# Kernel optimization log

Measured on AMD Instinct MI355X. Metric: run time of the kernel, lower is better.

The kernel has to match this reference:

```python
import jax, jax.numpy as jnp
import numpy as np

K = 3  # Chebyshev order (number of coefficients)


def setup_inputs() -> dict:
    key = jax.random.key(0)
    k1, k2, k3, k4 = jax.random.split(key, 4)
    B, nNode, c_in, T = 16, 512, 32, 64
    c_out = 64
    x = jax.random.normal(k1, (B, nNode, c_in, T), dtype=jnp.float32)
    # scaled Laplacian-like batched adjacency; scale keeps the Chebyshev
    # recursion numerically tame (spectral norm ~ O(1))
    adj = jax.random.normal(k2, (B, nNode, nNode), dtype=jnp.float32) * (1.0 / np.sqrt(nNode))
    # 1x1 conv params: weight [c_out, K*c_in], bias [c_out]
    W = jax.random.normal(k3, (c_out, K * c_in), dtype=jnp.float32) * 0.1
    b = jax.random.normal(k4, (c_out,), dtype=jnp.float32) * 0.1
    return {"x": x, "adj": adj, "W": W, "b": b}


def reference(x, adj, W, b):
    # x: [B, nNode, c_in, T] -> permute(0,2,1,3) -> [B, c_in, nNode, T]
    x = jnp.transpose(x, (0, 2, 1, 3))
    B, c_in, nNode, T = x.shape
    # Chebyshev recursion: L0 = I, L1 = adj, L_k = 2*adj@L_{k-1} - L_{k-2}
    L0 = jnp.broadcast_to(jnp.eye(nNode, dtype=x.dtype), (B, nNode, nNode))
    L1 = adj
    Ls = [L0, L1]
    for _ in range(2, K):
        L2 = 2.0 * jnp.matmul(adj, L1) - L0
        L0, L1 = L1, L2
        Ls.append(L2)
    Lap = jnp.stack(Ls, axis=1)              # [B, K, nNode, nNode]
    Lap = jnp.swapaxes(Lap, -1, -2)          # transpose(-1, -2)
    # einsum 'bcnl,bknq->bckql' then view [B, c_in*K, nNode, T]
    y = jnp.einsum('bcnl,bknq->bckql', x, Lap)  # [B, c_in, K, nNode, T]
    y = y.reshape(B, c_in * K, nNode, T)
    # 1x1 Conv2d: channel mixing + bias
    out = jnp.einsum('oc,bcnl->bonl', W, y) + b[None, :, None, None]
    return out
```

## Files before the change

kernel.cpp:

```cpp
#include <hip/hip_runtime.h>

typedef unsigned short u16;
typedef __bf16 v8bf __attribute__((ext_vector_type(8)));
typedef float f32x4 __attribute__((ext_vector_type(4)));
typedef float f32x16 __attribute__((ext_vector_type(16)));
typedef u16 us8 __attribute__((ext_vector_type(8)));
typedef u16 us4 __attribute__((ext_vector_type(4)));

static __device__ __forceinline__ u16 f2bf(float f) {
  union { __bf16 h; u16 u; } cv;
  cv.h = (__bf16)f;
  return cv.u;
}

static __device__ __forceinline__ void gl_lds16(const u16* g, u16* l) {
  __builtin_amdgcn_global_load_lds(
      (const __attribute__((address_space(1))) unsigned int*)g,
      (__attribute__((address_space(3))) unsigned int*)l, 16, 0, 0);
}

__global__ __launch_bounds__(256)
void prep_k(const float* __restrict__ adj, u16* __restrict__ adjC,
            u16* __restrict__ adjT_bf, const float* __restrict__ x,
            u16* __restrict__ xT, const float* __restrict__ W,
            u16* __restrict__ Mb) {
  const int bid = blockIdx.x;
  const int tid = threadIdx.x;
  __shared__ u16 Ls[64][68];
  if (bid < 1024) {
    const int b = bid >> 6;
    const int r0 = ((bid >> 3) & 7) * 64;
    const int c0 = (bid & 7) * 64;
#pragma unroll
    for (int i = 0; i < 4; ++i) {
      const int idx = tid + 256 * i;
      const int r = idx >> 4;
      const int c4 = (idx & 15) * 4;
      const float4 v = *(const float4*)(adj + ((size_t)(b * 512 + r0 + r) * 512 + c0 + c4));
      us4 o;
      o[0] = f2bf(v.x); o[1] = f2bf(v.y); o[2] = f2bf(v.z); o[3] = f2bf(v.w);
      *(us4*)&Ls[r][c4] = o;
      *(us4*)(adjC + ((size_t)(b * 1024 + r0 + r) * 512 + c0 + c4)) = o;
    }
    __syncthreads();
#pragma unroll
    for (int i = 0; i < 2; ++i) {
      const int idx = tid + 256 * i;
      const int c = idx >> 3;
      const int r8 = (idx & 7) * 8;
      us8 o;
#pragma unroll
      for (int j = 0; j < 8; ++j) o[j] = Ls[r8 + j][c];
      *(us8*)(adjT_bf + ((size_t)(b * 512 + c0 + c) * 512 + r0 + r8)) = o;
    }
  } else if (bid < 5120) {
    const int t = bid - 1024;
    const int b = t >> 8;
    const int q0 = ((t >> 5) & 7) * 64;
    const int j0 = (t & 31) * 64;
#pragma unroll
    for (int i = 0; i < 4; ++i) {
      const int idx = tid + 256 * i;
      const int r = idx >> 4;
      const int j4 = (idx & 15) * 4;
      const float4 v = *(const float4*)(x + ((size_t)(b * 512 + q0 + r) * 2048 + j0 + j4));
      us4 o;
      o[0] = f2bf(v.x); o[1] = f2bf(v.y); o[2] = f2bf(v.z); o[3] = f2bf(v.w);
      *(us4*)&Ls[r][j4] = o;
    }
    __syncthreads();
#pragma unroll
    for (int i = 0; i < 2; ++i) {
      const int idx = tid + 256 * i;
      const int jp = idx >> 3;
      const int q8 = (idx & 7) * 8;
      us8 o;
#pragma unroll
      for (int j = 0; j < 8; ++j) o[j] = Ls[q8 + j][jp];
      *(us8*)(xT + ((size_t)(b * 2048 + j0 + jp) * 512 + q0 + q8)) = o;
    }
  } else {
    for (int i = tid; i < 64 * 96; i += 256) {
      const int cc = i % 96;
      const int r = cc % 3;
      const float w = W[i];
      const float m = (r == 0) ? (w - W[i + 2]) : w;
      Mb[i] = f2bf(m);
    }
  }
}

__global__ __launch_bounds__(256)
void gemm_sq(const u16* __restrict__ adjC_in, const u16* __restrict__ BT,
             u16* __restrict__ adjC) {
  const int b = blockIdx.z;
  const int row0 = blockIdx.y * 128;
  const int col0 = blockIdx.x * 128;
  const u16* Ab = adjC_in + (size_t)b * 1024 * 512;
  const u16* BTb = BT + (size_t)b * 512 * 512;

  __shared__ u16 smem[16384];
  u16* As = smem;
  u16* Bs = smem + 8192;

  const int tid = threadIdx.x;
  const int lane = tid & 63;
  const int w = tid >> 6;
  const int wm = (w >> 1) * 64;
  const int wn = (w & 1) * 64;
  const int l16 = lane & 15;
  const int kg = lane >> 4;

  f32x4 acc[4][4];
#pragma unroll
  for (int m = 0; m < 4; ++m)
#pragma unroll
    for (int n = 0; n < 4; ++n) acc[m][n] = (f32x4){0.f, 0.f, 0.f, 0.f};

  for (int k0 = 0; k0 < 512; k0 += 64) {
    __syncthreads();
#pragma unroll
    for (int i = 0; i < 4; ++i) {
      const int eb = w * 2048 + i * 512;
      const int e = eb + lane * 8;
      const int r = e >> 6;
      const int kk = e & 63;
      gl_lds16(Ab + (size_t)(row0 + r) * 512 + k0 + kk, As + eb);
      gl_lds16(BTb + (size_t)(col0 + r) * 512 + k0 + kk, Bs + eb);
    }
    __syncthreads();
#pragma unroll
    for (int ks = 0; ks < 2; ++ks) {
      v8bf af[4], bfr[4];
#pragma unroll
      for (int m = 0; m < 4; ++m)
        af[m] = *(const v8bf*)(As + (wm + m * 16 + l16) * 64 + ks * 32 + kg * 8);
#pragma unroll
      for (int n = 0; n < 4; ++n)
        bfr[n] = *(const v8bf*)(Bs + (wn + n * 16 + l16) * 64 + ks * 32 + kg * 8);
#pragma unroll
      for (int m = 0; m < 4; ++m)
#pragma unroll
        for (int n = 0; n < 4; ++n)
          acc[m][n] = __builtin_amdgcn_mfma_f32_16x16x32_bf16(af[m], bfr[n], acc[m][n], 0, 0, 0);
    }
  }
  u16* Cb = adjC + (size_t)b * 1024 * 512 + (size_t)512 * 512;
#pragma unroll
  for (int m = 0; m < 4; ++m)
#pragma unroll
    for (int n = 0; n < 4; ++n)
#pragma unroll
      for (int v = 0; v < 4; ++v) {
        const int rr = row0 + wm + m * 16 + kg * 4 + v;
        const int cc = col0 + wn + n * 16 + l16;
        Cb[(size_t)rr * 512 + cc] = f2bf(2.0f * acc[m][n][v]);
      }
}

__global__ __launch_bounds__(512)
void prop_k(const u16* __restrict__ AC, const u16* __restrict__ BT,
            u16* __restrict__ C) {
  const int fid = blockIdx.x + 16 * (blockIdx.y + 4 * blockIdx.z);
  const int wk = (fid & 7) * 128 + (fid >> 3);
  const int b = wk >> 6;
  const int row0 = ((wk >> 4) & 3) * 256;
  const int col0 = (wk & 15) * 128;
  const u16* Ab = AC + (size_t)b * 1024 * 512;
  const u16* BTb = BT + (size_t)b * 2048 * 512;

  __shared__ u16 smem[24576];
  u16* As = smem;
  u16* Bs = smem + 16384;

  const int tid = threadIdx.x;
  const int lane = tid & 63;
  const int w = tid >> 6;
  const int wm = (w >> 1) * 64;
  const int wn = (w & 1) * 64;
  const int l32 = lane & 31;
  const int hk = lane >> 5;
  const int rsw = (l32 & 7) << 3;

  f32x16 acc[2][2];
#pragma unroll
  for (int mi = 0; mi < 2; ++mi)
#pragma unroll
    for (int ni = 0; ni < 2; ++ni)
#pragma unroll
      for (int v = 0; v < 16; ++v) acc[mi][ni][v] = 0.f;

  for (int k0 = 0; k0 < 512; k0 += 64) {
    __syncthreads();
#pragma unroll
    for (int i = 0; i < 4; ++i) {
      const int cb = w * 64 + i * 512;
      const int c = cb + lane;
      const int r = c >> 3;
      const int slot = (c & 7) ^ (r & 7);
      gl_lds16(Ab + (size_t)(row0 + r) * 512 + k0 + slot * 8, As + cb * 8);
    }
#pragma unroll
    for (int i = 0; i < 2; ++i) {
      const int cb = w * 64 + i * 512;
      const int c = cb + lane;
      const int r = c >> 3;
      const int slot = (c & 7) ^ (r & 7);
      gl_lds16(BTb + (size_t)(col0 + r) * 512 + k0 + slot * 8, Bs + cb * 8);
    }
    __syncthreads();
#pragma unroll
    for (int ks = 0; ks < 4; ++ks) {
      v8bf af[2], bf[2];
#pragma unroll
      for (int mi = 0; mi < 2; ++mi) {
        const int row = wm + mi * 32 + l32;
        af[mi] = *(const v8bf*)(As + row * 64 + ((ks * 16 + hk * 8) ^ rsw));
      }
#pragma unroll
      for (int ni = 0; ni < 2; ++ni) {
        const int row = wn + ni * 32 + l32;
        bf[ni] = *(const v8bf*)(Bs + row * 64 + ((ks * 16 + hk * 8) ^ rsw));
      }
#pragma unroll
      for (int mi = 0; mi < 2; ++mi)
#pragma unroll
        for (int ni = 0; ni < 2; ++ni)
          acc[mi][ni] = __builtin_amdgcn_mfma_f32_32x32x16_bf16(af[mi], bf[ni], acc[mi][ni], 0, 0, 0);
    }
  }

  u16* Cb = C + (size_t)b * 1024 * 2048;
#pragma unroll
  for (int mi = 0; mi < 2; ++mi)
#pragma unroll
    for (int ni = 0; ni < 2; ++ni)
#pragma unroll
      for (int r = 0; r < 16; ++r) {
        const int rr = row0 + wm + mi * 32 + (r & 3) + 8 * (r >> 2) + 4 * hk;
        const int cc = col0 + wn + ni * 32 + l32;
        Cb[(size_t)rr * 2048 + cc] = f2bf(acc[mi][ni][r]);
      }
}

__global__ __launch_bounds__(256)
void mix_mfma(const float* __restrict__ x0, const u16* __restrict__ X1Y2,
              const u16* __restrict__ Mb, const float* __restrict__ bias,
              float* __restrict__ out) {
  const int q = blockIdx.x;
  const int b = blockIdx.y;
  __shared__ u16 Vt[64][104];
  __shared__ u16 Ms[64][104];
  const int tid = threadIdx.x;
  const int lane = tid & 63;
  const int w = tid >> 6;
  const int l16 = lane & 15;
  const int kg = lane >> 4;

#pragma unroll
  for (int i = 0; i < 3; ++i) {
    const int idx = tid + 256 * i;
    const int o = idx / 12;
    const int c8 = (idx % 12) * 8;
    *(uint4*)&Ms[o][c8] = *(const uint4*)(Mb + o * 96 + c8);
  }
  const size_t base0 = ((size_t)b * 512 + q) * 2048;
  const size_t base1 = ((size_t)b * 1024 + q) * 2048;
  const size_t base2 = ((size_t)b * 1024 + 512 + q) * 2048;
#pragma unroll
  for (int i = 0; i < 2; ++i) {
    const int idx = tid + 256 * i;
    const int c = idx >> 4;
    const int l0 = (idx & 15) * 4;
    const float4 v = *(const float4*)(x0 + base0 + c * 64 + l0);
    Vt[l0 + 0][3 * c] = f2bf(v.x);
    Vt[l0 + 1][3 * c] = f2bf(v.y);
    Vt[l0 + 2][3 * c] = f2bf(v.z);
    Vt[l0 + 3][3 * c] = f2bf(v.w);
  }
  {
    const int c = tid >> 3;
    const int l0 = (tid & 7) * 8;
    const us8 v1 = *(const us8*)(X1Y2 + base1 + c * 64 + l0);
    const us8 v2 = *(const us8*)(X1Y2 + base2 + c * 64 + l0);
#pragma unroll
    for (int j = 0; j < 8; ++j) {
      Vt[l0 + j][3 * c + 1] = v1[j];
      Vt[l0 + j][3 * c + 2] = v2[j];
    }
  }
  __syncthreads();

  f32x4 acc[4];
#pragma unroll
  for (int n = 0; n < 4; ++n) acc[n] = (f32x4){0.f, 0.f, 0.f, 0.f};
#pragma unroll
  for (int ks = 0; ks < 3; ++ks) {
    const v8bf a = *(const v8bf*)&Ms[w * 16 + l16][ks * 32 + kg * 8];
#pragma unroll
    for (int n = 0; n < 4; ++n) {
      const v8bf bv = *(const v8bf*)&Vt[n * 16 + l16][ks * 32 + kg * 8];
      acc[n] = __builtin_amdgcn_mfma_f32_16x16x32_bf16(a, bv, acc[n], 0, 0, 0);
    }
  }
#pragma unroll
  for (int n = 0; n < 4; ++n)
#pragma unroll
    for (int v = 0; v < 4; ++v) {
      const int o = w * 16 + kg * 4 + v;
      out[(((size_t)b * 64 + o) * 512 + q) * 64 + n * 16 + l16] = acc[n][v] + bias[o];
    }
}

extern "C" void kernel_launch(void* const* d_in, const int* in_sizes, int n_in,
                              void* d_out, int out_size, void* d_ws, size_t ws_size,
                              hipStream_t stream) {
  const float* x   = (const float*)d_in[0];
  const float* adj = (const float*)d_in[1];
  const float* W   = (const float*)d_in[2];
  const float* bia = (const float*)d_in[3];
  float* out = (float*)d_out;

  u16* adjC    = (u16*)d_ws;
  u16* adjT_bf = adjC    + (size_t)16 * 1024 * 512;
  u16* xT      = adjT_bf + (size_t)16 * 512 * 512;
  u16* X1Y2    = xT      + (size_t)16 * 2048 * 512;
  u16* Mb      = X1Y2    + (size_t)16 * 1024 * 2048;

  hipLaunchKernelGGL(prep_k, dim3(5121), dim3(256), 0, stream,
                     adj, adjC, adjT_bf, x, xT, W, Mb);
  hipLaunchKernelGGL(gemm_sq, dim3(4, 4, 16), dim3(256), 0, stream,
                     adjC, adjT_bf, adjC);
  hipLaunchKernelGGL(prop_k, dim3(16, 4, 16), dim3(512), 0, stream,
                     adjC, xT, X1Y2);
  hipLaunchKernelGGL(mix_mfma, dim3(512, 16), dim3(256), 0, stream,
                     x, X1Y2, Mb, bia, out);
}
```

Baseline: 135.8 us.

## Fuse x transpose and bf16 conversion into propagation GEMM B-tile load

Drops the separate prep pass that transposed x into a bf16 xT buffer. prop_k now reads fp32 x directly with strided per-thread loads, converts to bf16 in registers, and writes the swizzled B tile into LDS. This avoids writing and re-reading a 32 MB bf16 intermediate. In exchange the GEMM main loop now issues synchronous strided global loads instead of async global-to-LDS copies, and each x element is reread by the 4 row blocks per batch.

```diff
diff --git a/kernel.cpp b/kernel.cpp
--- a/kernel.cpp
+++ b/kernel.cpp
@@ -21,8 +21,7 @@
 
 __global__ __launch_bounds__(256)
 void prep_k(const float* __restrict__ adj, u16* __restrict__ adjC,
-            u16* __restrict__ adjT_bf, const float* __restrict__ x,
-            u16* __restrict__ xT, const float* __restrict__ W,
+            u16* __restrict__ adjT_bf, const float* __restrict__ W,
             u16* __restrict__ Mb) {
   const int bid = blockIdx.x;
   const int tid = threadIdx.x;
@@ -53,32 +52,6 @@
       for (int j = 0; j < 8; ++j) o[j] = Ls[r8 + j][c];
       *(us8*)(adjT_bf + ((size_t)(b * 512 + c0 + c) * 512 + r0 + r8)) = o;
     }
-  } else if (bid < 5120) {
-    const int t = bid - 1024;
-    const int b = t >> 8;
-    const int q0 = ((t >> 5) & 7) * 64;
-    const int j0 = (t & 31) * 64;
-#pragma unroll
-    for (int i = 0; i < 4; ++i) {
-      const int idx = tid + 256 * i;
-      const int r = idx >> 4;
-      const int j4 = (idx & 15) * 4;
-      const float4 v = *(const float4*)(x + ((size_t)(b * 512 + q0 + r) * 2048 + j0 + j4));
-      us4 o;
-      o[0] = f2bf(v.x); o[1] = f2bf(v.y); o[2] = f2bf(v.z); o[3] = f2bf(v.w);
-      *(us4*)&Ls[r][j4] = o;
-    }
-    __syncthreads();
-#pragma unroll
-    for (int i = 0; i < 2; ++i) {
-      const int idx = tid + 256 * i;
-      const int jp = idx >> 3;
-      const int q8 = (idx & 7) * 8;
-      us8 o;
-#pragma unroll
-      for (int j = 0; j < 8; ++j) o[j] = Ls[q8 + j][jp];
-      *(us8*)(xT + ((size_t)(b * 2048 + j0 + jp) * 512 + q0 + q8)) = o;
-    }
   } else {
     for (int i = tid; i < 64 * 96; i += 256) {
       const int cc = i % 96;
@@ -159,7 +132,7 @@
 }
 
 __global__ __launch_bounds__(512)
-void prop_k(const u16* __restrict__ AC, const u16* __restrict__ BT,
+void prop_k(const u16* __restrict__ AC, const float* __restrict__ X,
             u16* __restrict__ C) {
   const int fid = blockIdx.x + 16 * (blockIdx.y + 4 * blockIdx.z);
   const int wk = (fid & 7) * 128 + (fid >> 3);
@@ -167,7 +140,7 @@
   const int row0 = ((wk >> 4) & 3) * 256;
   const int col0 = (wk & 15) * 128;
   const u16* Ab = AC + (size_t)b * 1024 * 512;
-  const u16* BTb = BT + (size_t)b * 2048 * 512;
+  const float* Xb = X + (size_t)b * 512 * 2048;
 
   __shared__ u16 smem[24576];
   u16* As = smem;
@@ -181,6 +154,8 @@
   const int l32 = lane & 31;
   const int hk = lane >> 5;
   const int rsw = (l32 & 7) << 3;
+  const int jj = tid & 127;
+  const int qg = tid >> 7;
 
   f32x16 acc[2][2];
 #pragma unroll
@@ -202,11 +177,15 @@
     }
 #pragma unroll
     for (int i = 0; i < 2; ++i) {
-      const int cb = w * 64 + i * 512;
-      const int c = cb + lane;
-      const int r = c >> 3;
-      const int slot = (c & 7) ^ (r & 7);
-      gl_lds16(BTb + (size_t)(col0 + r) * 512 + k0 + slot * 8, Bs + cb * 8);
+      const int oct = qg + i * 4;
+      const float* src = Xb + (size_t)(k0 + oct * 8) * 2048 + col0 + jj;
+      float v[8];
+#pragma unroll
+      for (int u = 0; u < 8; ++u) v[u] = src[(size_t)u * 2048];
+      us8 o;
+#pragma unroll
+      for (int u = 0; u < 8; ++u) o[u] = f2bf(v[u]);
+      *(us8*)(Bs + jj * 64 + ((oct ^ (jj & 7)) * 8)) = o;
     }
     __syncthreads();
 #pragma unroll
@@ -323,16 +302,15 @@
 
   u16* adjC    = (u16*)d_ws;
   u16* adjT_bf = adjC    + (size_t)16 * 1024 * 512;
-  u16* xT      = adjT_bf + (size_t)16 * 512 * 512;
-  u16* X1Y2    = xT      + (size_t)16 * 2048 * 512;
+  u16* X1Y2    = adjT_bf + (size_t)16 * 512 * 512;
   u16* Mb      = X1Y2    + (size_t)16 * 1024 * 2048;
 
-  hipLaunchKernelGGL(prep_k, dim3(5121), dim3(256), 0, stream,
-                     adj, adjC, adjT_bf, x, xT, W, Mb);
+  hipLaunchKernelGGL(prep_k, dim3(1025), dim3(256), 0, stream,
+                     adj, adjC, adjT_bf, W, Mb);
   hipLaunchKernelGGL(gemm_sq, dim3(4, 4, 16), dim3(256), 0, stream,
                      adjC, adjT_bf, adjC);
   hipLaunchKernelGGL(prop_k, dim3(16, 4, 16), dim3(512), 0, stream,
-                     adjC, xT, X1Y2);
+                     adjC, x, X1Y2);
   hipLaunchKernelGGL(mix_mfma, dim3(512, 16), dim3(256), 0, stream,
                      x, X1Y2, Mb, bia, out);
 }
```

Result: slower. 149.0 us (+9.7%).

## Overlap adjacency squaring GEMM with x transpose in one launch

Applied to the files above, without the earlier changes.

Moves the x bf16 transpose out of the prep kernel into the same launch as the adj@adj GEMM, so the 256 GEMM blocks and the 4096 transpose blocks run together. Before, the GEMM launch had only 256 blocks and left much of the GPU idle. The prep kernel now handles only the adjacency conversion and weight folding, so it is smaller. The trade-off is that the combined kernel shares one shared-memory size and register budget across both roles, which can hurt occupancy for the transpose blocks.

```diff
diff --git a/kernel.cpp b/kernel.cpp
--- a/kernel.cpp
+++ b/kernel.cpp
@@ -20,10 +20,9 @@
 }
 
 __global__ __launch_bounds__(256)
-void prep_k(const float* __restrict__ adj, u16* __restrict__ adjC,
-            u16* __restrict__ adjT_bf, const float* __restrict__ x,
-            u16* __restrict__ xT, const float* __restrict__ W,
-            u16* __restrict__ Mb) {
+void prep_adj_k(const float* __restrict__ adj, u16* __restrict__ adjC,
+                u16* __restrict__ adjT_bf, const float* __restrict__ W,
+                u16* __restrict__ Mb) {
   const int bid = blockIdx.x;
   const int tid = threadIdx.x;
   __shared__ u16 Ls[64][68];
@@ -53,8 +52,89 @@
       for (int j = 0; j < 8; ++j) o[j] = Ls[r8 + j][c];
       *(us8*)(adjT_bf + ((size_t)(b * 512 + c0 + c) * 512 + r0 + r8)) = o;
     }
-  } else if (bid < 5120) {
-    const int t = bid - 1024;
+  } else {
+    for (int i = tid; i < 64 * 96; i += 256) {
+      const int cc = i % 96;
+      const int r = cc % 3;
+      const float w = W[i];
+      const float m = (r == 0) ? (w - W[i + 2]) : w;
+      Mb[i] = f2bf(m);
+    }
+  }
+}
+
+__global__ __launch_bounds__(256)
+void phase2_k(const u16* __restrict__ adjC_in, const u16* __restrict__ BT,
+              u16* __restrict__ adjC, const float* __restrict__ x,
+              u16* __restrict__ xT) {
+  const int bid = blockIdx.x;
+  const int tid = threadIdx.x;
+  __shared__ u16 smem[16384];
+  if (bid < 256) {
+    const int b = bid >> 4;
+    const int row0 = ((bid >> 2) & 3) * 128;
+    const int col0 = (bid & 3) * 128;
+    const u16* Ab = adjC_in + (size_t)b * 1024 * 512;
+    const u16* BTb = BT + (size_t)b * 512 * 512;
+
+    u16* As = smem;
+    u16* Bs = smem + 8192;
+
+    const int lane = tid & 63;
+    const int w = tid >> 6;
+    const int wm = (w >> 1) * 64;
+    const int wn = (w & 1) * 64;
+    const int l16 = lane & 15;
+    const int kg = lane >> 4;
+
+    f32x4 acc[4][4];
+#pragma unroll
+    for (int m = 0; m < 4; ++m)
+#pragma unroll
+      for (int n = 0; n < 4; ++n) acc[m][n] = (f32x4){0.f, 0.f, 0.f, 0.f};
+
+    for (int k0 = 0; k0 < 512; k0 += 64) {
+      __syncthreads();
+#pragma unroll
+      for (int i = 0; i < 4; ++i) {
+        const int eb = w * 2048 + i * 512;
+        const int e = eb + lane * 8;
+        const int r = e >> 6;
+        const int kk = e & 63;
+        gl_lds16(Ab + (size_t)(row0 + r) * 512 + k0 + kk, As + eb);
+        gl_lds16(BTb + (size_t)(col0 + r) * 512 + k0 + kk, Bs + eb);
+      }
+      __syncthreads();
+#pragma unroll
+      for (int ks = 0; ks < 2; ++ks) {
+        v8bf af[4], bfr[4];
+#pragma unroll
+        for (int m = 0; m < 4; ++m)
+          af[m] = *(const v8bf*)(As + (wm + m * 16 + l16) * 64 + ks * 32 + kg * 8);
+#pragma unroll
+        for (int n = 0; n < 4; ++n)
+          bfr[n] = *(const v8bf*)(Bs + (wn + n * 16 + l16) * 64 + ks * 32 + kg * 8);
+#pragma unroll
+        for (int m = 0; m < 4; ++m)
+#pragma unroll
+          for (int n = 0; n < 4; ++n)
+            acc[m][n] = __builtin_amdgcn_mfma_f32_16x16x32_bf16(af[m], bfr[n], acc[m][n], 0, 0, 0);
+      }
+    }
+    u16* Cb = adjC + (size_t)b * 1024 * 512 + (size_t)512 * 512;
+#pragma unroll
+    for (int m = 0; m < 4; ++m)
+#pragma unroll
+      for (int n = 0; n < 4; ++n)
+#pragma unroll
+        for (int v = 0; v < 4; ++v) {
+          const int rr = row0 + wm + m * 16 + kg * 4 + v;
+          const int cc = col0 + wn + n * 16 + l16;
+          Cb[(size_t)rr * 512 + cc] = f2bf(2.0f * acc[m][n][v]);
+        }
+  } else {
+    u16 (*Ls)[68] = (u16(*)[68])smem;
+    const int t = bid - 256;
     const int b = t >> 8;
     const int q0 = ((t >> 5) & 7) * 64;
     const int j0 = (t & 31) * 64;
@@ -79,83 +159,7 @@
       for (int j = 0; j < 8; ++j) o[j] = Ls[q8 + j][jp];
       *(us8*)(xT + ((size_t)(b * 2048 + j0 + jp) * 512 + q0 + q8)) = o;
     }
-  } else {
-    for (int i = tid; i < 64 * 96; i += 256) {
-      const int cc = i % 96;
-      const int r = cc % 3;
-      const float w = W[i];
-      const float m = (r == 0) ? (w - W[i + 2]) : w;
-      Mb[i] = f2bf(m);
-    }
-  }
-}
-
-__global__ __launch_bounds__(256)
-void gemm_sq(const u16* __restrict__ adjC_in, const u16* __restrict__ BT,
-             u16* __restrict__ adjC) {
-  const int b = blockIdx.z;
-  const int row0 = blockIdx.y * 128;
-  const int col0 = blockIdx.x * 128;
-  const u16* Ab = adjC_in + (size_t)b * 1024 * 512;
-  const u16* BTb = BT + (size_t)b * 512 * 512;
-
-  __shared__ u16 smem[16384];
-  u16* As = smem;
-  u16* Bs = smem + 8192;
-
-  const int tid = threadIdx.x;
-  const int lane = tid & 63;
-  const int w = tid >> 6;
-  const int wm = (w >> 1) * 64;
-  const int wn = (w & 1) * 64;
-  const int l16 = lane & 15;
-  const int kg = lane >> 4;
-
-  f32x4 acc[4][4];
-#pragma unroll
-  for (int m = 0; m < 4; ++m)
-#pragma unroll
-    for (int n = 0; n < 4; ++n) acc[m][n] = (f32x4){0.f, 0.f, 0.f, 0.f};
-
-  for (int k0 = 0; k0 < 512; k0 += 64) {
-    __syncthreads();
-#pragma unroll
-    for (int i = 0; i < 4; ++i) {
-      const int eb = w * 2048 + i * 512;
-      const int e = eb + lane * 8;
-      const int r = e >> 6;
-      const int kk = e & 63;
-      gl_lds16(Ab + (size_t)(row0 + r) * 512 + k0 + kk, As + eb);
-      gl_lds16(BTb + (size_t)(col0 + r) * 512 + k0 + kk, Bs + eb);
-    }
-    __syncthreads();
-#pragma unroll
-    for (int ks = 0; ks < 2; ++ks) {
-      v8bf af[4], bfr[4];
-#pragma unroll
-      for (int m = 0; m < 4; ++m)
-        af[m] = *(const v8bf*)(As + (wm + m * 16 + l16) * 64 + ks * 32 + kg * 8);
-#pragma unroll
-      for (int n = 0; n < 4; ++n)
-        bfr[n] = *(const v8bf*)(Bs + (wn + n * 16 + l16) * 64 + ks * 32 + kg * 8);
-#pragma unroll
-      for (int m = 0; m < 4; ++m)
-#pragma unroll
-        for (int n = 0; n < 4; ++n)
-          acc[m][n] = __builtin_amdgcn_mfma_f32_16x16x32_bf16(af[m], bfr[n], acc[m][n], 0, 0, 0);
-    }
-  }
-  u16* Cb = adjC + (size_t)b * 1024 * 512 + (size_t)512 * 512;
-#pragma unroll
-  for (int m = 0; m < 4; ++m)
-#pragma unroll
-    for (int n = 0; n < 4; ++n)
-#pragma unroll
-      for (int v = 0; v < 4; ++v) {
-        const int rr = row0 + wm + m * 16 + kg * 4 + v;
-        const int cc = col0 + wn + n * 16 + l16;
-        Cb[(size_t)rr * 512 + cc] = f2bf(2.0f * acc[m][n][v]);
-      }
+  }
 }
 
 __global__ __launch_bounds__(512)
@@ -327,10 +331,10 @@
   u16* X1Y2    = xT      + (size_t)16 * 2048 * 512;
   u16* Mb      = X1Y2    + (size_t)16 * 1024 * 2048;
 
-  hipLaunchKernelGGL(prep_k, dim3(5121), dim3(256), 0, stream,
-                     adj, adjC, adjT_bf, x, xT, W, Mb);
-  hipLaunchKernelGGL(gemm_sq, dim3(4, 4, 16), dim3(256), 0, stream,
-                     adjC, adjT_bf, adjC);
+  hipLaunchKernelGGL(prep_adj_k, dim3(1025), dim3(256), 0, stream,
+                     adj, adjC, adjT_bf, W, Mb);
+  hipLaunchKernelGGL(phase2_k, dim3(4352), dim3(256), 0, stream,
+                     adjC, adjT_bf, adjC, x, xT);
   hipLaunchKernelGGL(prop_k, dim3(16, 4, 16), dim3(512), 0, stream,
                      adjC, xT, X1Y2);
   hipLaunchKernelGGL(mix_mfma, dim3(512, 16), dim3(256), 0, stream,
```

After: 133.7 us. About the same (-1.5%).
